# Kernel tuning notes

Hardware: AMD Instinct MI355X
Metric: run time of the kernel (lower is better)

The kernel has to match this reference:

```python
import jax, jax.numpy as jnp
import numpy as np

N_NODES = 100000
N_EDGES = 800000
# (in_dim, out_channels_per_head, heads) for the 5 stacked GATConv layers
DIMS = [(32, 24, 10), (240, 24, 5), (120, 24, 2), (48, 24, 1), (24, 12, 1)]
NEG_SLOPE = 0.2  # PyG GATConv default leaky_relu slope


def setup_inputs() -> dict:
    key = jax.random.key(0)
    ks = jax.random.split(key, 4 + 4 * len(DIMS))
    x = jax.random.normal(ks[0], (N_NODES, 32), jnp.float32)
    # edge_index with no self loops (dst = src + nonzero offset mod N),
    # since PyG GATConv removes then re-adds self loops.
    src = jax.random.randint(ks[1], (N_EDGES,), 0, N_NODES)
    off = jax.random.randint(ks[2], (N_EDGES,), 1, N_NODES)
    dst = (src + off) % N_NODES
    edge_index = jnp.stack([src, dst]).astype(jnp.int32)
    edge_attr = jax.random.normal(ks[3], (N_EDGES, 4), jnp.float32)
    inp = {"x": x, "edge_index": edge_index, "edge_attr": edge_attr}
    for i, (din, c, h) in enumerate(DIMS):
        kw, kb, ka, kd = ks[4 + 4 * i: 8 + 4 * i]
        s = 1.0 / np.sqrt(din)
        inp[f"W{i}"] = jax.random.normal(kw, (din, h * c), jnp.float32) * s
        inp[f"b{i}"] = jax.random.normal(kb, (h * c,), jnp.float32) * 0.01
        inp[f"as{i}"] = jax.random.normal(ka, (h, c), jnp.float32) * (1.0 / np.sqrt(c))
        inp[f"ad{i}"] = jax.random.normal(kd, (h, c), jnp.float32) * (1.0 / np.sqrt(c))
    return inp


def gat_layer(x, src, dst, W, b, a_src, a_dst):
    # Faithful PyG GATConv (concat=True, bias=True, edge_dim=None)
    n = x.shape[0]
    h_heads, c = a_src.shape
    h = (x @ W).reshape(n, h_heads, c)                      # [N,H,C]
    alpha_s = jnp.einsum('nhc,hc->nh', h, a_src)            # [N,H]
    alpha_d = jnp.einsum('nhc,hc->nh', h, a_dst)            # [N,H]
    e = jax.nn.leaky_relu(alpha_s[src] + alpha_d[dst], NEG_SLOPE)  # [E,H]
    # segment softmax over incoming edges of each destination node
    m = jax.ops.segment_max(e, dst, num_segments=n)         # [N,H]
    ex = jnp.exp(e - m[dst])
    z = jax.ops.segment_sum(ex, dst, num_segments=n)        # [N,H]
    attn = ex / z[dst]                                      # [E,H]
    out = jax.ops.segment_sum(h[src] * attn[:, :, None], dst, num_segments=n)
    return out.reshape(n, h_heads * c) + b


def reference(x, edge_index, edge_attr,
              W0, b0, as0, ad0, W1, b1, as1, ad1, W2, b2, as2, ad2,
              W3, b3, as3, ad3, W4, b4, as4, ad4):
    # edge_attr is ignored: GATConv(edge_dim=None) does not use it.
    n = x.shape[0]
    loop = jnp.arange(n, dtype=edge_index.dtype)
    src = jnp.concatenate([edge_index[0], loop])  # add self loops (PyG default)
    dst = jnp.concatenate([edge_index[1], loop])
    params = [(W0, b0, as0, ad0), (W1, b1, as1, ad1), (W2, b2, as2, ad2),
              (W3, b3, as3, ad3), (W4, b4, as4, ad4)]
    for W, b, a_s, a_d in params:
        x = jax.nn.relu(gat_layer(x, src, dst, W, b, a_s, a_d))
    return x
```

## Files before the change

kernel.cpp:

```cpp
#include <hip/hip_runtime.h>
#include <math.h>

#define NN 100000
#define EE 800000
#define ET (EE + NN)
#define BS 256
#define BKTS 391
#define FB_EPB 4096
#define LDSCAP 4096
#define DBINS 64

typedef _Float16 f16;
typedef __attribute__((ext_vector_type(2))) _Float16 h2v;
typedef __attribute__((ext_vector_type(4))) _Float16 half4;
typedef __attribute__((ext_vector_type(8))) _Float16 half8;
typedef __attribute__((ext_vector_type(4))) float f32x4;
template<int V> struct HV;
template<> struct HV<4>{ typedef half4 type; };
template<> struct HV<8>{ typedef half8 type; };

static inline int cdiv(long a, int b){ return (int)((a + b - 1) / b); }

__global__ __launch_bounds__(256) void k_bhist(const int* __restrict__ ei,
                                               int* __restrict__ bucketCount){
    __shared__ int hist[BKTS];
    for (int t = threadIdx.x; t < BKTS; t += 256) hist[t] = 0;
    __syncthreads();
    const int e0 = blockIdx.x * FB_EPB + threadIdx.x;
    #pragma unroll
    for (int i = 0; i < 16; i++){
        int e = e0 + i * 256;
        if (e < ET){
            int d = (e < EE) ? ei[EE + e] : (e - EE);
            atomicAdd(&hist[d >> 8], 1);
        }
    }
    __syncthreads();
    for (int t = threadIdx.x; t < BKTS; t += 256){
        int c = hist[t];
        if (c) atomicAdd(&bucketCount[t], c);
    }
}

__global__ void k_bscan(const int* __restrict__ bucketCount, int* __restrict__ bucketBase,
                        int* __restrict__ bucketCursor, int* __restrict__ rowptr){
    __shared__ int sh[512];
    int t = threadIdx.x;
    int c = (t < BKTS) ? bucketCount[t] : 0;
    sh[t] = c;
    __syncthreads();
    for (int o = 1; o < 512; o <<= 1){
        int v = (t >= o) ? sh[t - o] : 0;
        __syncthreads();
        sh[t] += v;
        __syncthreads();
    }
    if (t < BKTS){
        int excl = sh[t] - c;
        bucketBase[t] = excl;
        bucketCursor[t] = excl;
    }
    if (t == 0){
        bucketBase[BKTS] = ET;
        rowptr[NN] = ET;
    }
}

__global__ __launch_bounds__(256) void k_bfill(const int* __restrict__ ei,
        int* __restrict__ bucketCursor, unsigned* __restrict__ bpack){
    __shared__ int hist[BKTS];
    __shared__ int base[BKTS];
    for (int t = threadIdx.x; t < BKTS; t += 256) hist[t] = 0;
    __syncthreads();
    const int e0 = blockIdx.x * FB_EPB + threadIdx.x;
    unsigned pk[16], rb[16];
    #pragma unroll
    for (int i = 0; i < 16; i++){
        int e = e0 + i * 256;
        rb[i] = 0xFFFFFFFFu;
        if (e < ET){
            int s, d;
            if (e < EE){ s = ei[e]; d = ei[EE + e]; } else { s = e - EE; d = s; }
            int b = d >> 8;
            int r = atomicAdd(&hist[b], 1);
            pk[i] = ((unsigned)(d & 255) << 17) | (unsigned)s;
            rb[i] = ((unsigned)r << 9) | (unsigned)b;
        }
    }
    __syncthreads();
    for (int t = threadIdx.x; t < BKTS; t += 256){
        int c = hist[t];
        base[t] = c ? atomicAdd(&bucketCursor[t], c) : 0;
    }
    __syncthreads();
    #pragma unroll
    for (int i = 0; i < 16; i++){
        if (rb[i] != 0xFFFFFFFFu){
            int b = rb[i] & 511;
            int r = rb[i] >> 9;
            bpack[base[b] + r] = pk[i];
        }
    }
}

__global__ __launch_bounds__(256) void k_bsort(const unsigned* __restrict__ bpack,
        const int* __restrict__ bucketBase, int* __restrict__ rowptr,
        int* __restrict__ ssrc){
    __shared__ int cnt[256];
    __shared__ int off[256];
    __shared__ unsigned stage[LDSCAP];
    int b = blockIdx.x;
    int n0 = bucketBase[b], n1 = bucketBase[b + 1];
    int nE = n1 - n0;
    int t = threadIdx.x;
    cnt[t] = 0;
    __syncthreads();
    for (int i = t; i < nE; i += 256){
        unsigned v = bpack[n0 + i];
        atomicAdd(&cnt[v >> 17], 1);
    }
    __syncthreads();
    int cv = cnt[t];
    off[t] = cv;
    __syncthreads();
    for (int o = 1; o < 256; o <<= 1){
        int v = (t >= o) ? off[t - o] : 0;
        __syncthreads();
        off[t] += v;
        __syncthreads();
    }
    int excl = off[t] - cv;
    __syncthreads();
    off[t] = excl;
    cnt[t] = 0;
    __syncthreads();
    for (int i = t; i < nE; i += 256){
        unsigned v = bpack[n0 + i];
        int dl = v >> 17;
        int r = atomicAdd(&cnt[dl], 1);
        stage[off[dl] + r] = v;
    }
    int d = b * 256 + t;
    if (d < NN) rowptr[d] = n0 + excl;
    __syncthreads();
    for (int i = t; i < nE; i += 256){
        unsigned v = stage[i];
        ssrc[n0 + i] = (int)(v & 0x1FFFFu);
    }
}

__global__ __launch_bounds__(256) void k_dhist(const int* __restrict__ rowptr,
                                               int* __restrict__ dcnt){
    __shared__ int h[DBINS];
    int t = threadIdx.x;
    if (t < DBINS) h[t] = 0;
    __syncthreads();
    int n = blockIdx.x * 256 + t;
    if (n < NN){
        int d = rowptr[n + 1] - rowptr[n];
        if (d > DBINS - 1) d = DBINS - 1;
        atomicAdd(&h[d], 1);
    }
    __syncthreads();
    if (t < DBINS && h[t]) atomicAdd(&dcnt[t], h[t]);
}

__global__ void k_dscan(const int* __restrict__ dcnt, int* __restrict__ dcur){
    __shared__ int sh[DBINS];
    int t = threadIdx.x;
    sh[t] = dcnt[t];
    __syncthreads();
    int off = 0;
    for (int b = t + 1; b < DBINS; ++b) off += sh[b];
    dcur[t] = off;
}

__global__ __launch_bounds__(256) void k_dfill(const int* __restrict__ rowptr,
        int* __restrict__ dcur, int* __restrict__ perm){
    __shared__ int h[DBINS];
    __shared__ int base[DBINS];
    int t = threadIdx.x;
    if (t < DBINS) h[t] = 0;
    __syncthreads();
    int n = blockIdx.x * 256 + t;
    int d = 0, r = 0;
    if (n < NN){
        d = rowptr[n + 1] - rowptr[n];
        if (d > DBINS - 1) d = DBINS - 1;
        r = atomicAdd(&h[d], 1);
    }
    __syncthreads();
    if (t < DBINS){
        int c = h[t];
        base[t] = c ? atomicAdd(&dcur[t], c) : 0;
    }
    __syncthreads();
    if (n < NN) perm[base[d] + r] = n;
}

template<int K, int M, int KP, int MP, int HH, int CC>
__device__ __forceinline__ void prep_one(int idx, const float* __restrict__ W,
        const float* __restrict__ b, const float* __restrict__ as_,
        const float* __restrict__ ad_, f16* __restrict__ Wpk,
        float* __restrict__ bp, float* __restrict__ Was, float* __restrict__ Wad){
    constexpr int NT = MP / 16;
    if (idx < KP * MP){
        int j    = idx & 7;
        int lane = (idx >> 3) & 63;
        int rest = idx >> 9;
        int nt   = rest % NT;
        int ks   = rest / NT;
        int k = ks * 32 + ((lane >> 4) & 3) * 8 + j;
        int n = nt * 16 + (lane & 15);
        Wpk[idx] = (k < K && n < M) ? (f16)W[k * M + n] : (f16)0.f;
    }
    if (idx < MP) bp[idx] = (idx < M) ? b[idx] : 0.f;
    if (idx < K * HH){
        int k = idx / HH, hd = idx - k * HH;
        float s = 0.f, d = 0.f;
        #pragma unroll
        for (int c = 0; c < CC; c++){
            float w = W[k * M + hd * CC + c];
            s = fmaf(w, as_[hd * CC + c], s);
            d = fmaf(w, ad_[hd * CC + c], d);
        }
        Was[idx] = s;
        Wad[idx] = d;
    }
}

__device__ __forceinline__ void prep_w0(int idx, const float* __restrict__ W0,
                                        f16* __restrict__ Wpk0){
    int j    = idx & 7;
    int lane = (idx >> 3) & 63;
    int nt   = (idx >> 9) & 1;
    int hd   = idx >> 10;
    int k    = ((lane >> 4) & 3) * 8 + j;
    int cih  = nt * 16 + (lane & 15);
    Wpk0[idx] = (cih < 24) ? (f16)W0[k * 240 + hd * 24 + cih] : (f16)0.f;
}

struct PrepAll {
    const float *W[5], *b[5], *as[5], *ad[5];
    f16*   Wpk[5];
    f16*   Wpk0;
    float* bp[5];
    float* Was[5];
    float* Wad[5];
    int*   bucketCount;
    int*   dcnt;
};

__global__ void k_prep_all(PrepAll a){
    int idx = blockIdx.x * 256 + threadIdx.x;
    if (idx < 7680)
        prep_one< 32, 240,  32, 240, 10, 24>(idx,         a.W[0], a.b[0], a.as[0], a.ad[0], a.Wpk[0], a.bp[0], a.Was[0], a.Wad[0]);
    else if (idx < 40448)
        prep_one<240, 120, 256, 128,  5, 24>(idx - 7680,  a.W[1], a.b[1], a.as[1], a.ad[1], a.Wpk[1], a.bp[1], a.Was[1], a.Wad[1]);
    else if (idx < 48640)
        prep_one<120,  48, 128,  64,  2, 24>(idx - 40448, a.W[2], a.b[2], a.as[2], a.ad[2], a.Wpk[2], a.bp[2], a.Was[2], a.Wad[2]);
    else if (idx < 50688)
        prep_one< 48,  24,  64,  32,  1, 24>(idx - 48640, a.W[3], a.b[3], a.as[3], a.ad[3], a.Wpk[3], a.bp[3], a.Was[3], a.Wad[3]);
    else if (idx < 51200)
        prep_one< 24,  12,  32,  16,  1, 12>(idx - 50688, a.W[4], a.b[4], a.as[4], a.ad[4], a.Wpk[4], a.bp[4], a.Was[4], a.Wad[4]);
    else if (idx < 61440)
        prep_w0(idx - 51200, a.W[0], a.Wpk0);
    else if (idx < 61440 + BKTS)
        a.bucketCount[idx - 61440] = 0;
    else if (idx < 61440 + BKTS + DBINS)
        a.dcnt[idx - 61440 - BKTS] = 0;
}

__global__ void k_cvt_alpha0(const float* __restrict__ X, f16* __restrict__ Xh,
                             const float* __restrict__ Was, const float* __restrict__ Wad,
                             float* __restrict__ als, float* __restrict__ ald){
    int n = blockIdx.x * BS + threadIdx.x;
    if (n >= NN) return;
    float xr[32];
    #pragma unroll
    for (int i = 0; i < 8; i++){
        float4 v = *(const float4*)(X + (long)n * 32 + i * 4);
        xr[i * 4 + 0] = v.x; xr[i * 4 + 1] = v.y;
        xr[i * 4 + 2] = v.z; xr[i * 4 + 3] = v.w;
    }
    #pragma unroll
    for (int i = 0; i < 4; i++){
        half8 h;
        #pragma unroll
        for (int c = 0; c < 8; c++) h[c] = (f16)xr[i * 8 + c];
        *(half8*)(Xh + (long)n * 32 + i * 8) = h;
    }
    float s[10] = {}, d[10] = {};
    for (int k = 0; k < 32; k++){
        float x = xr[k];
        #pragma unroll
        for (int hd = 0; hd < 10; hd++){
            s[hd] = fmaf(x, Was[k * 10 + hd], s[hd]);
            d[hd] = fmaf(x, Wad[k * 10 + hd], d[hd]);
        }
    }
    #pragma unroll
    for (int hd = 0; hd < 10; hd++){
        als[(long)n * 12 + hd] = s[hd];
        ald[(long)n * 12 + hd] = d[hd];
    }
}

template<int MPH, int HH, int CC, int SL>
__global__ void k_alpha_h(const f16* __restrict__ H2, const float* __restrict__ as_,
                          const float* __restrict__ ad_, float* __restrict__ als,
                          float* __restrict__ ald){
    int n = blockIdx.x * BS + threadIdx.x;
    if (n >= NN) return;
    const f16* h = H2 + (long)n * MPH;
    #pragma unroll
    for (int hd = 0; hd < HH; hd++){
        float s = 0.f, d = 0.f;
        #pragma unroll
        for (int c0 = 0; c0 < CC; c0 += 4){
            half4 hv = *(const half4*)(h + hd * CC + c0);
            #pragma unroll
            for (int j = 0; j < 4; j++){
                float hvf = (float)hv[j];
                s = fmaf(hvf, as_[hd * CC + c0 + j], s);
                d = fmaf(hvf, ad_[hd * CC + c0 + j], d);
            }
        }
        als[(long)n * SL + hd] = s;
        ald[(long)n * SL + hd] = d;
    }
}

__device__ __forceinline__ void smx_upd(float& ma, float& L, float& z, float e, float adv){
    float mn = fmaxf(ma, e);
    float Ln = mn + adv; Ln = (Ln >= 0.f) ? Ln : 0.2f * Ln;
    float ev = e + adv;  ev = (ev >= 0.f) ? ev : 0.2f * ev;
    z = z * __expf(L - Ln) + __expf(ev - Ln);
    ma = mn; L = Ln;
}

template<int HH, int SL, int ATTS, int TPN>
__global__ __launch_bounds__(256) void k_mzatt_split(const float* __restrict__ als,
        const float* __restrict__ ald, const int* __restrict__ rowptr,
        const int* __restrict__ ssrc, f16* __restrict__ att){
    constexpr int HPT = HH / TPN;
    long idx = (long)blockIdx.x * 256 + threadIdx.x;
    if (idx >= (long)NN * TPN) return;
    int n = (int)(idx / TPN);
    int g = (int)(idx - (long)n * TPN);
    const int c0 = g * HPT;
    float adv[HPT], ma[HPT], L[HPT], z[HPT];
    #pragma unroll
    for (int h = 0; h < HPT; h++){
        adv[h] = ald[(long)n * SL + c0 + h];
        ma[h] = -1e30f; L[h] = -1e30f; z[h] = 0.f;
    }
    const int beg = rowptr[n], end = rowptr[n + 1];
    int p = beg;
    for (; p + 4 <= end; p += 4){
        int s0 = ssrc[p], s1 = ssrc[p+1], s2 = ssrc[p+2], s3 = ssrc[p+3];
        float e0[HPT], e1[HPT], e2[HPT], e3[HPT];
        if constexpr (HPT == 2){
            float2 v0 = *(const float2*)(als + (long)s0 * SL + c0);
            float2 v1 = *(const float2*)(als + (long)s1 * SL + c0);
            float2 v2 = *(const float2*)(als + (long)s2 * SL + c0);
            float2 v3 = *(const float2*)(als + (long)s3 * SL + c0);
            e0[0]=v0.x; e0[1]=v0.y; e1[0]=v1.x; e1[1]=v1.y;
            e2[0]=v2.x; e2[1]=v2.y; e3[0]=v3.x; e3[1]=v3.y;
        } else {
            e0[0] = als[(long)s0 * SL + c0];
            e1[0] = als[(long)s1 * SL + c0];
            e2[0] = als[(long)s2 * SL + c0];
            e3[0] = als[(long)s3 * SL + c0];
        }
        #pragma unroll
        for (int h = 0; h < HPT; h++){
            smx_upd(ma[h], L[h], z[h], e0[h], adv[h]);
            smx_upd(ma[h], L[h], z[h], e1[h], adv[h]);
            smx_upd(ma[h], L[h], z[h], e2[h], adv[h]);
            smx_upd(ma[h], L[h], z[h], e3[h], adv[h]);
        }
    }
    for (; p < end; ++p){
        int s = ssrc[p];
        float e[HPT];
        if constexpr (HPT == 2){
            float2 v = *(const float2*)(als + (long)s * SL + c0);
            e[0] = v.x; e[1] = v.y;
        } else {
            e[0] = als[(long)s * SL + c0];
        }
        #pragma unroll
        for (int h = 0; h < HPT; h++) smx_upd(ma[h], L[h], z[h], e[h], adv[h]);
    }
    float zi[HPT];
    int pos[HPT];
    #pragma unroll
    for (int h = 0; h < HPT; h++){
        zi[h] = 1.f / z[h];
        int hh = c0 + h;
        pos[h] = (ATTS == 16) ? (hh + ((hh >= 5) ? 3 : 0)) : hh;
    }
    auto emit = [&](int pp, const float* e){
        #pragma unroll
        for (int h = 0; h < HPT; h++){
            float ev = e[h] + adv[h]; ev = (ev >= 0.f) ? ev : 0.2f * ev;
            att[(long)pp * ATTS + pos[h]] = (f16)(__expf(ev - L[h]) * zi[h]);
        }
    };
    p = beg;
    for (; p + 4 <= end; p += 4){
        int s0 = ssrc[p], s1 = ssrc[p+1], s2 = ssrc[p+2], s3 = ssrc[p+3];
        float e0[HPT], e1[HPT], e2[HPT], e3[HPT];
        if constexpr (HPT == 2){
            float2 v0 = *(const float2*)(als + (long)s0 * SL + c0);
            float2 v1 = *(const float2*)(als + (long)s1 * SL + c0);
            float2 v2 = *(const float2*)(als + (long)s2 * SL + c0);
            float2 v3 = *(const float2*)(als + (long)s3 * SL + c0);
            e0[0]=v0.x; e0[1]=v0.y; e1[0]=v1.x; e1[1]=v1.y;
            e2[0]=v2.x; e2[1]=v2.y; e3[0]=v3.x; e3[1]=v3.y;
        } else {
            e0[0] = als[(long)s0 * SL + c0];
            e1[0] = als[(long)s1 * SL + c0];
            e2[0] = als[(long)s2 * SL + c0];
            e3[0] = als[(long)s3 * SL + c0];
        }
        emit(p, e0); emit(p+1, e1); emit(p+2, e2); emit(p+3, e3);
    }
    for (; p < end; ++p){
        int s = ssrc[p];
        float e[HPT];
        if constexpr (HPT == 2){
            float2 v = *(const float2*)(als + (long)s * SL + c0);
            e[0] = v.x; e[1] = v.y;
        } else {
            e[0] = als[(long)s * SL + c0];
        }
        emit(p, e);
    }
}

__global__ __launch_bounds__(256) void k_aggX0_gemm(const f16* __restrict__ Xh,
        const f16* __restrict__ att, const int* __restrict__ rowptr,
        const int* __restrict__ ssrc, const int* __restrict__ perm,
        const f16* __restrict__ Wpk0, const float* __restrict__ bp0,
        f16* __restrict__ X1){
    constexpr int SA = 328;
    constexpr int SO = 264;
    __shared__ f16 smem[32 * SA];
    const int t = threadIdx.x;
    const int n0 = blockIdx.x * 32;

    {
        const int nloc = t >> 3;
        const int hg   = (t >> 2) & 1;
        const int ch   = t & 3;
        const int n    = perm[n0 + nloc];
        float acc[5][8] = {};
        int beg = rowptr[n], end = rowptr[n + 1];
        int p = beg;
        for (; p + 4 <= end; p += 4){
            int s0 = ssrc[p], s1 = ssrc[p+1], s2 = ssrc[p+2], s3 = ssrc[p+3];
            half8 x0 = *(const half8*)(Xh + (long)s0 * 32 + ch * 8);
            half8 x1 = *(const half8*)(Xh + (long)s1 * 32 + ch * 8);
            half8 x2 = *(const half8*)(Xh + (long)s2 * 32 + ch * 8);
            half8 x3 = *(const half8*)(Xh + (long)s3 * 32 + ch * 8);
            half8 a0 = *(const half8*)(att + (long)p * 16 + hg * 8);
            half8 a1 = *(const half8*)(att + (long)(p+1) * 16 + hg * 8);
            half8 a2 = *(const half8*)(att + (long)(p+2) * 16 + hg * 8);
            half8 a3 = *(const half8*)(att + (long)(p+3) * 16 + hg * 8);
            #pragma unroll
            for (int h = 0; h < 5; h++){
                float w0 = (float)a0[h], w1 = (float)a1[h];
                float w2 = (float)a2[h], w3 = (float)a3[h];
                #pragma unroll
                for (int c = 0; c < 8; c++){
                    acc[h][c] = fmaf(w0, (float)x0[c], acc[h][c]);
                    acc[h][c] = fmaf(w1, (float)x1[c], acc[h][c]);
                    acc[h][c] = fmaf(w2, (float)x2[c], acc[h][c]);
                    acc[h][c] = fmaf(w3, (float)x3[c], acc[h][c]);
                }
            }
        }
        for (; p < end; ++p){
            int s = ssrc[p];
            half8 xv = *(const half8*)(Xh + (long)s * 32 + ch * 8);
            half8 av = *(const half8*)(att + (long)p * 16 + hg * 8);
            #pragma unroll
            for (int h = 0; h < 5; h++){
                float w = (float)av[h];
                #pragma unroll
                for (int c = 0; c < 8; c++)
                    acc[h][c] = fmaf(w, (float)xv[c], acc[h][c]);
            }
        }
        #pragma unroll
        for (int h = 0; h < 5; h++){
            half8 o;
            #pragma unroll
            for (int c = 0; c < 8; c++) o[c] = (f16)acc[h][c];
            *(half8*)(smem + nloc * SA + (hg * 5 + h) * 32 + ch * 8) = o;
        }
    }
    __syncthreads();

    const int wave = t >> 6;
    const int lane = t & 63;
    const int quad = lane >> 4;
    const int l16  = lane & 15;
    const int mt   = wave & 1;
    half8 afr[5];
    #pragma unroll
    for (int i = 0; i < 5; i++){
        const int hd = (wave + 4 * i) >> 1;
        afr[i] = *(const half8*)(smem + (mt * 16 + l16) * SA + hd * 32 + quad * 8);
    }
    __syncthreads();
    #pragma unroll
    for (int i = 0; i < 5; i++){
        const int hd = (wave + 4 * i) >> 1;
        #pragma unroll
        for (int nt = 0; nt < 2; nt++){
            half8 bfr = *(const half8*)(Wpk0 + ((hd * 2 + nt) * 64 + lane) * 8);
            f32x4 acc2 = (f32x4){0.f, 0.f, 0.f, 0.f};
            acc2 = __builtin_amdgcn_mfma_f32_16x16x32_f16(afr[i], bfr, acc2, 0, 0, 0);
            int cih = nt * 16 + l16;
            if (cih < 24){
                float bv = bp0[hd * 24 + cih];
                #pragma unroll
                for (int reg = 0; reg < 4; reg++){
                    int rl = mt * 16 + quad * 4 + reg;
                    float v = acc2[reg] + bv;
                    smem[rl * SO + hd * 24 + cih] = (f16)((v > 0.f) ? v : 0.f);
                }
            }
        }
    }
    __syncthreads();

    const half8 hz = {};
    #pragma unroll
    for (int c = t; c < 1024; c += 256){
        int row = c >> 5, c8 = c & 31;
        long rn = perm[n0 + row];
        half8 v = (c8 >= 30) ? hz : *(const half8*)(smem + row * SO + c8 * 8);
        *(half8*)(X1 + rn * 256 + c8 * 8) = v;
    }
}

template<int KP, int MPH>
__global__ __launch_bounds__(256) void k_gemm_mfma(const f16* __restrict__ Xh,
        const f16* __restrict__ Wpk, f16* __restrict__ H2){
    constexpr int NT = MPH / 16;
    constexpr int KS = KP / 32;
    const int wave = threadIdx.x >> 6;
    const int lane = threadIdx.x & 63;
    const int quad = lane >> 4;
    const int l16  = lane & 15;
    const long row0 = (long)blockIdx.x * 128 + wave * 32;

    f32x4 acc[2][NT];
    #pragma unroll
    for (int mt = 0; mt < 2; mt++)
        #pragma unroll
        for (int nt = 0; nt < NT; nt++)
            acc[mt][nt] = (f32x4){0.f, 0.f, 0.f, 0.f};

    const long r0 = row0 + l16;
    const long r1 = row0 + 16 + l16;
    const half8 hz = {};
    half8 a0 = (r0 < NN) ? *(const half8*)(Xh + r0 * KP + quad * 8) : hz;
    half8 a1 = (r1 < NN) ? *(const half8*)(Xh + r1 * KP + quad * 8) : hz;
    half8 bc[NT];
    #pragma unroll
    for (int nt = 0; nt < NT; nt++)
        bc[nt] = *(const half8*)(Wpk + ((long)nt * 64 + lane) * 8);

    for (int ks = 0; ks < KS; ks++){
        half8 n0 = hz, n1 = hz, bn[NT];
        if (ks + 1 < KS){
            const int kk = (ks + 1) * 32 + quad * 8;
            n0 = (r0 < NN) ? *(const half8*)(Xh + r0 * KP + kk) : hz;
            n1 = (r1 < NN) ? *(const half8*)(Xh + r1 * KP + kk) : hz;
            const f16* bp_ = Wpk + ((long)(ks + 1) * NT * 64 + lane) * 8;
            #pragma unroll
            for (int nt = 0; nt < NT; nt++)
                bn[nt] = *(const half8*)(bp_ + (long)nt * 512);
        } else {
            #pragma unroll
            for (int nt = 0; nt < NT; nt++) bn[nt] = hz;
        }
        #pragma unroll
        for (int nt = 0; nt < NT; nt++){
            acc[0][nt] = __builtin_amdgcn_mfma_f32_16x16x32_f16(a0, bc[nt], acc[0][nt], 0, 0, 0);
            acc[1][nt] = __builtin_amdgcn_mfma_f32_16x16x32_f16(a1, bc[nt], acc[1][nt], 0, 0, 0);
        }
        a0 = n0; a1 = n1;
        #pragma unroll
        for (int nt = 0; nt < NT; nt++) bc[nt] = bn[nt];
    }
    #pragma unroll
    for (int mt = 0; mt < 2; mt++){
        #pragma unroll
        for (int reg = 0; reg < 4; reg++){
            long r = row0 + mt * 16 + quad * 4 + reg;
            if (r < NN){
                #pragma unroll
                for (int nt = 0; nt < NT; nt++)
                    H2[r * MPH + nt * 16 + l16] = (f16)acc[mt][nt][reg];
            }
        }
    }
}

template<int HH, int CC, int ATTS, int MPH, int MPO, int VEC, bool O16>
__global__ __launch_bounds__(256) void k_agg_h(const f16* __restrict__ H2,
        const f16* __restrict__ att,
        const int* __restrict__ rowptr, const int* __restrict__ ssrc,
        const float* __restrict__ bp, f16* __restrict__ out16,
        float* __restrict__ out32, int MREAL){
    constexpr int TPN = MPO / VEC;
    typedef typename HV<VEC>::type hvec;
    int idx = blockIdx.x * 256 + threadIdx.x;
    if (idx >= NN * TPN) return;
    int n = idx / TPN;
    int q = idx - n * TPN;
    int j0 = q * VEC;
    if constexpr (O16 && (MPO > MPH)){
        if (j0 >= MPH){
            hvec zv = {};
            *(hvec*)(out16 + (long)n * MPO + j0) = zv;
            return;
        }
    }
    int hd = j0 / CC; if (hd > HH - 1) hd = HH - 1;

    int beg = rowptr[n], end = rowptr[n + 1];
    float acc[VEC] = {};
    int p = beg;
    for (; p + 4 <= end; p += 4){
        int s0 = ssrc[p], s1 = ssrc[p+1], s2 = ssrc[p+2], s3 = ssrc[p+3];
        float w0 = (float)att[(long)p * ATTS + hd];
        float w1 = (float)att[(long)(p+1) * ATTS + hd];
        float w2 = (float)att[(long)(p+2) * ATTS + hd];
        float w3 = (float)att[(long)(p+3) * ATTS + hd];
        hvec h0 = *(const hvec*)(H2 + (long)s0 * MPH + j0);
        hvec h1 = *(const hvec*)(H2 + (long)s1 * MPH + j0);
        hvec h2 = *(const hvec*)(H2 + (long)s2 * MPH + j0);
        hvec h3 = *(const hvec*)(H2 + (long)s3 * MPH + j0);
        #pragma unroll
        for (int c = 0; c < VEC; c++){
            acc[c] = fmaf(w0, (float)h0[c], acc[c]);
            acc[c] = fmaf(w1, (float)h1[c], acc[c]);
            acc[c] = fmaf(w2, (float)h2[c], acc[c]);
            acc[c] = fmaf(w3, (float)h3[c], acc[c]);
        }
    }
    for (; p < end; ++p){
        int s = ssrc[p];
        float w = (float)att[(long)p * ATTS + hd];
        hvec hv = *(const hvec*)(H2 + (long)s * MPH + j0);
        #pragma unroll
        for (int c = 0; c < VEC; c++)
            acc[c] = fmaf(w, (float)hv[c], acc[c]);
    }
    if constexpr (O16){
        hvec o;
        #pragma unroll
        for (int c = 0; c < VEC; c++){
            float v = acc[c] + bp[j0 + c];
            o[c] = (f16)((v > 0.f) ? v : 0.f);
        }
        *(hvec*)(out16 + (long)n * MPO + j0) = o;
    } else {
        if (j0 < MREAL){
            #pragma unroll
            for (int c = 0; c < VEC; c++){
                float v = acc[c] + bp[j0 + c];
                out32[(long)n * MREAL + j0 + c] = (v > 0.f) ? v : 0.f;
            }
        }
    }
}

template<int K, int M, int KP, int MPH, int MPO, int HH, int CC, int ATTS, int VEC,
         bool O16, int SL, int TPN>
static void run_layer(const f16* Xin, f16* H2, f16* att,
                      const f16* Wpk, const float* bp,
                      const float* asv, const float* adv,
                      float* als, float* ald,
                      const int* rowptr, const int* ssrc,
                      f16* Xnext, float* out32, hipStream_t stream){
    constexpr int OTPN = MPO / VEC;
    k_gemm_mfma<KP, MPH><<<cdiv(NN, 128), 256, 0, stream>>>(Xin, Wpk, H2);
    k_alpha_h<MPH, HH, CC, SL><<<cdiv(NN, BS), BS, 0, stream>>>(H2, asv, adv, als, ald);
    k_mzatt_split<HH, SL, ATTS, TPN><<<cdiv((long)NN * TPN, 256), 256, 0, stream>>>(
        als, ald, rowptr, ssrc, att);
    k_agg_h<HH, CC, ATTS, MPH, MPO, VEC, O16><<<cdiv((long)NN * OTPN, 256), 256, 0, stream>>>(
        H2, att, rowptr, ssrc, bp, Xnext, out32, M);
}

extern "C" void kernel_launch(void* const* d_in, const int* in_sizes, int n_in,
                              void* d_out, int out_size, void* d_ws, size_t ws_size,
                              hipStream_t stream){
    const float* x0 = (const float*)d_in[0];
    const int*   ei = (const int*)d_in[1];
    PrepAll pa;
    for (int i = 0; i < 5; i++){
        pa.W[i]  = (const float*)d_in[3 + 4 * i];
        pa.b[i]  = (const float*)d_in[4 + 4 * i];
        pa.as[i] = (const float*)d_in[5 + 4 * i];
        pa.ad[i] = (const float*)d_in[6 + 4 * i];
    }

    char* p = (char*)d_ws;
    auto alloc = [&](size_t bytes) -> char* {
        char* r = p;
        p += (bytes + 255) & ~(size_t)255;
        return r;
    };
    f16*   Xh     = (f16*)alloc((size_t)NN * 256 * 2);
    f16*   H2     = (f16*)alloc((size_t)NN * 320 * 2);
    f16*   att    = (f16*)alloc((size_t)ET * 16 * 2);
    float* als    = (float*)alloc((size_t)NN * 12 * 4);
    float* ald    = (float*)alloc((size_t)NN * 12 * 4);
    const int wpkSz[5] = {7680, 32768, 8192, 2048, 512};
    const int mpSz[5]  = {240, 128, 64, 32, 16};
    const int khSz[5]  = {320, 1200, 240, 48, 24};
    for (int i = 0; i < 5; i++){
        pa.Wpk[i] = (f16*)alloc((size_t)wpkSz[i] * 2);
        pa.bp[i]  = (float*)alloc((size_t)mpSz[i] * 4);
        pa.Was[i] = (float*)alloc((size_t)khSz[i] * 4);
        pa.Wad[i] = (float*)alloc((size_t)khSz[i] * 4);
    }
    pa.Wpk0 = (f16*)alloc((size_t)10240 * 2);
    int*      bucketCount  = (int*)alloc((size_t)BKTS * 4);
    int*      bucketBase   = (int*)alloc((size_t)(BKTS + 1) * 4);
    int*      bucketCursor = (int*)alloc((size_t)BKTS * 4);
    unsigned* bpack        = (unsigned*)alloc((size_t)ET * 4);
    int*      rowptr       = (int*)alloc((size_t)(NN + 1) * 4);
    int*      ssrc         = (int*)alloc((size_t)ET * 4);
    int*      dcnt         = (int*)alloc((size_t)DBINS * 4);
    int*      dcur         = (int*)alloc((size_t)DBINS * 4);
    int*      perm         = (int*)alloc((size_t)NN * 4);
    pa.bucketCount = bucketCount;
    pa.dcnt = dcnt;

    k_prep_all<<<242, 256, 0, stream>>>(pa);
    k_bhist<<<cdiv(ET, FB_EPB), 256, 0, stream>>>(ei, bucketCount);
    k_bscan<<<1, 512, 0, stream>>>(bucketCount, bucketBase, bucketCursor, rowptr);
    k_bfill<<<cdiv(ET, FB_EPB), 256, 0, stream>>>(ei, bucketCursor, bpack);
    k_bsort<<<BKTS, 256, 0, stream>>>(bpack, bucketBase, rowptr, ssrc);
    k_dhist<<<cdiv(NN, 256), 256, 0, stream>>>(rowptr, dcnt);
    k_dscan<<<1, DBINS, 0, stream>>>(dcnt, dcur);
    k_dfill<<<cdiv(NN, 256), 256, 0, stream>>>(rowptr, dcur, perm);

    k_cvt_alpha0<<<cdiv(NN, BS), BS, 0, stream>>>(x0, Xh, pa.Was[0], pa.Wad[0], als, ald);
    k_mzatt_split<10, 12, 16, 5><<<cdiv((long)NN * 5, 256), 256, 0, stream>>>(
        als, ald, rowptr, ssrc, att);
    k_aggX0_gemm<<<NN / 32, 256, 0, stream>>>(Xh, att, rowptr, ssrc, perm,
        pa.Wpk0, pa.bp[0], H2 );

    run_layer<240, 120, 256, 128, 128,  5, 24, 8, 8, true,  8, 5>(H2, Xh, att, pa.Wpk[1],
        pa.bp[1], pa.as[1], pa.ad[1], als, ald, rowptr, ssrc, H2, nullptr, stream);
    run_layer<120,  48, 128,  64,  64,  2, 24, 2, 8, true,  2, 2>(H2, Xh, att, pa.Wpk[2],
        pa.bp[2], pa.as[2], pa.ad[2], als, ald, rowptr, ssrc, H2, nullptr, stream);
    run_layer< 48,  24,  64,  32,  32,  1, 24, 1, 8, true,  1, 1>(H2, Xh, att, pa.Wpk[3],
        pa.bp[3], pa.as[3], pa.ad[3], als, ald, rowptr, ssrc, H2, nullptr, stream);
    run_layer< 24,  12,  32,  16,  16,  1, 12, 1, 4, false, 1, 1>(H2, Xh, att, pa.Wpk[4],
        pa.bp[4], pa.as[4], pa.ad[4], als, ald, rowptr, ssrc, nullptr, (float*)d_out, stream);
}
```

Baseline: 465.0 us.

## Fuse segment softmax into aggregation and parallelize alpha projection for later layers

For layers 1-4, the separate softmax kernel that wrote per-edge attention weights is removed. The aggregation kernel now recomputes the online max and normalizer per node and head from the alpha values, then recomputes the weights while gathering features. This drops the attention write and re-read and one launch per layer, at the cost of every channel-group thread redoing the softmax gathers. The alpha projection now splits each node across threads and reduces in shared memory, and the degree histogram is folded into the bucket sort kernel so the k_dhist launch goes away.

```diff
diff --git a/kernel.cpp b/kernel.cpp
--- a/kernel.cpp
+++ b/kernel.cpp
@@ -11,7 +11,6 @@
 #define DBINS 64
 
 typedef _Float16 f16;
-typedef __attribute__((ext_vector_type(2))) _Float16 h2v;
 typedef __attribute__((ext_vector_type(4))) _Float16 half4;
 typedef __attribute__((ext_vector_type(8))) _Float16 half8;
 typedef __attribute__((ext_vector_type(4))) float f32x4;
@@ -105,7 +104,7 @@
 
 __global__ __launch_bounds__(256) void k_bsort(const unsigned* __restrict__ bpack,
         const int* __restrict__ bucketBase, int* __restrict__ rowptr,
-        int* __restrict__ ssrc){
+        int* __restrict__ ssrc, int* __restrict__ dcnt){
     __shared__ int cnt[256];
     __shared__ int off[256];
     __shared__ unsigned stage[LDSCAP];
@@ -141,28 +140,16 @@
         stage[off[dl] + r] = v;
     }
     int d = b * 256 + t;
-    if (d < NN) rowptr[d] = n0 + excl;
+    if (d < NN){
+        rowptr[d] = n0 + excl;
+        int dg = (cv > DBINS - 1) ? (DBINS - 1) : cv;
+        atomicAdd(&dcnt[dg], 1);
+    }
     __syncthreads();
     for (int i = t; i < nE; i += 256){
         unsigned v = stage[i];
         ssrc[n0 + i] = (int)(v & 0x1FFFFu);
     }
-}
-
-__global__ __launch_bounds__(256) void k_dhist(const int* __restrict__ rowptr,
-                                               int* __restrict__ dcnt){
-    __shared__ int h[DBINS];
-    int t = threadIdx.x;
-    if (t < DBINS) h[t] = 0;
-    __syncthreads();
-    int n = blockIdx.x * 256 + t;
-    if (n < NN){
-        int d = rowptr[n + 1] - rowptr[n];
-        if (d > DBINS - 1) d = DBINS - 1;
-        atomicAdd(&h[d], 1);
-    }
-    __syncthreads();
-    if (t < DBINS && h[t]) atomicAdd(&dcnt[t], h[t]);
 }
 
 __global__ void k_dscan(const int* __restrict__ dcnt, int* __restrict__ dcur){
@@ -306,28 +293,50 @@
     }
 }
 
-template<int MPH, int HH, int CC, int SL>
-__global__ void k_alpha_h(const f16* __restrict__ H2, const float* __restrict__ as_,
-                          const float* __restrict__ ad_, float* __restrict__ als,
-                          float* __restrict__ ald){
-    int n = blockIdx.x * BS + threadIdx.x;
-    if (n >= NN) return;
-    const f16* h = H2 + (long)n * MPH;
-    #pragma unroll
-    for (int hd = 0; hd < HH; hd++){
-        float s = 0.f, d = 0.f;
-        #pragma unroll
-        for (int c0 = 0; c0 < CC; c0 += 4){
-            half4 hv = *(const half4*)(h + hd * CC + c0);
+template<int MPH, int M, int HH, int CC, int SL>
+__global__ __launch_bounds__(256) void k_alpha_v2(const f16* __restrict__ H2,
+        const float* __restrict__ as_, const float* __restrict__ ad_,
+        float* __restrict__ als, float* __restrict__ ald){
+    constexpr int TA  = MPH / 8;
+    constexpr int NPB = 256 / TA;
+    __shared__ float sAs[256], sAd[256], sBs[256], sBd[256];
+    const int t  = threadIdx.x;
+    const int nl = t / TA;
+    const int c  = t - nl * TA;
+    const long n = (long)blockIdx.x * NPB + nl;
+    float pAs = 0.f, pAd = 0.f, pBs = 0.f, pBd = 0.f;
+    if (n < NN){
+        half8 hv = *(const half8*)(H2 + n * MPH + c * 8);
+        const int j0 = c * 8;
+        const int hA = j0 / CC;
+        const int sp = (hA + 1) * CC - j0;
+        #pragma unroll
+        for (int i = 0; i < 8; i++){
+            int j = j0 + i;
+            float w  = (float)hv[i];
+            float ws = (j < M) ? as_[j] : 0.f;
+            float wd = (j < M) ? ad_[j] : 0.f;
+            if (i < sp){ pAs = fmaf(w, ws, pAs); pAd = fmaf(w, wd, pAd); }
+            else       { pBs = fmaf(w, ws, pBs); pBd = fmaf(w, wd, pBd); }
+        }
+    }
+    sAs[t] = pAs; sAd[t] = pAd; sBs[t] = pBs; sBd[t] = pBd;
+    __syncthreads();
+    if (t < NPB * HH){
+        int nl2 = t / HH, hd = t - nl2 * HH;
+        long n2 = (long)blockIdx.x * NPB + nl2;
+        if (n2 < NN){
+            float s = 0.f, d = 0.f;
             #pragma unroll
-            for (int j = 0; j < 4; j++){
-                float hvf = (float)hv[j];
-                s = fmaf(hvf, as_[hd * CC + c0 + j], s);
-                d = fmaf(hvf, ad_[hd * CC + c0 + j], d);
+            for (int c2 = 0; c2 < TA; c2++){
+                int j0 = c2 * 8, hA = j0 / CC, sp = (hA + 1) * CC - j0;
+                int base = nl2 * TA + c2;
+                if (hA == hd){ s += sAs[base]; d += sAd[base]; }
+                if (sp < 8 && hA + 1 == hd){ s += sBs[base]; d += sBd[base]; }
             }
-        }
-        als[(long)n * SL + hd] = s;
-        ald[(long)n * SL + hd] = d;
+            als[n2 * SL + hd] = s;
+            ald[n2 * SL + hd] = d;
+        }
     }
 }
 
@@ -401,33 +410,7 @@
         int hh = c0 + h;
         pos[h] = (ATTS == 16) ? (hh + ((hh >= 5) ? 3 : 0)) : hh;
     }
-    auto emit = [&](int pp, const float* e){
-        #pragma unroll
-        for (int h = 0; h < HPT; h++){
-            float ev = e[h] + adv[h]; ev = (ev >= 0.f) ? ev : 0.2f * ev;
-            att[(long)pp * ATTS + pos[h]] = (f16)(__expf(ev - L[h]) * zi[h]);
-        }
-    };
-    p = beg;
-    for (; p + 4 <= end; p += 4){
-        int s0 = ssrc[p], s1 = ssrc[p+1], s2 = ssrc[p+2], s3 = ssrc[p+3];
-        float e0[HPT], e1[HPT], e2[HPT], e3[HPT];
-        if constexpr (HPT == 2){
-            float2 v0 = *(const float2*)(als + (long)s0 * SL + c0);
-            float2 v1 = *(const float2*)(als + (long)s1 * SL + c0);
-            float2 v2 = *(const float2*)(als + (long)s2 * SL + c0);
-            float2 v3 = *(const float2*)(als + (long)s3 * SL + c0);
-            e0[0]=v0.x; e0[1]=v0.y; e1[0]=v1.x; e1[1]=v1.y;
-            e2[0]=v2.x; e2[1]=v2.y; e3[0]=v3.x; e3[1]=v3.y;
-        } else {
-            e0[0] = als[(long)s0 * SL + c0];
-            e1[0] = als[(long)s1 * SL + c0];
-            e2[0] = als[(long)s2 * SL + c0];
-            e3[0] = als[(long)s3 * SL + c0];
-        }
-        emit(p, e0); emit(p+1, e1); emit(p+2, e2); emit(p+3, e3);
-    }
-    for (; p < end; ++p){
+    for (p = beg; p < end; ++p){
         int s = ssrc[p];
         float e[HPT];
         if constexpr (HPT == 2){
@@ -436,7 +419,11 @@
         } else {
             e[0] = als[(long)s * SL + c0];
         }
-        emit(p, e);
+        #pragma unroll
+        for (int h = 0; h < HPT; h++){
+            float ev = e[h] + adv[h]; ev = (ev >= 0.f) ? ev : 0.2f * ev;
+            att[(long)p * ATTS + pos[h]] = (f16)(__expf(ev - L[h]) * zi[h]);
+        }
     }
 }
 
@@ -613,37 +600,57 @@
     }
 }
 
-template<int HH, int CC, int ATTS, int MPH, int MPO, int VEC, bool O16>
-__global__ __launch_bounds__(256) void k_agg_h(const f16* __restrict__ H2,
-        const f16* __restrict__ att,
+template<int HH, int CC, int MPH, int MPO, int VEC, bool O16, int SL>
+__global__ __launch_bounds__(256) void k_aggsm_h(const f16* __restrict__ H2,
+        const float* __restrict__ als, const float* __restrict__ ald,
         const int* __restrict__ rowptr, const int* __restrict__ ssrc,
         const float* __restrict__ bp, f16* __restrict__ out16,
         float* __restrict__ out32, int MREAL){
     constexpr int TPN = MPO / VEC;
     typedef typename HV<VEC>::type hvec;
-    int idx = blockIdx.x * 256 + threadIdx.x;
-    if (idx >= NN * TPN) return;
-    int n = idx / TPN;
-    int q = idx - n * TPN;
+    long idx = (long)blockIdx.x * 256 + threadIdx.x;
+    if (idx >= (long)NN * TPN) return;
+    int n = (int)(idx / TPN);
+    int q = (int)(idx - (long)n * TPN);
     int j0 = q * VEC;
-    if constexpr (O16 && (MPO > MPH)){
-        if (j0 >= MPH){
-            hvec zv = {};
-            *(hvec*)(out16 + (long)n * MPO + j0) = zv;
-            return;
-        }
-    }
+    if constexpr (!O16){ if (j0 >= MREAL) return; }
     int hd = j0 / CC; if (hd > HH - 1) hd = HH - 1;
-
-    int beg = rowptr[n], end = rowptr[n + 1];
-    float acc[VEC] = {};
+    const float adv = ald[(long)n * SL + hd];
+    const int beg = rowptr[n], end = rowptr[n + 1];
+
+    float ma = -1e30f, L = -1e30f, z = 0.f;
     int p = beg;
     for (; p + 4 <= end; p += 4){
         int s0 = ssrc[p], s1 = ssrc[p+1], s2 = ssrc[p+2], s3 = ssrc[p+3];
-        float w0 = (float)att[(long)p * ATTS + hd];
-        float w1 = (float)att[(long)(p+1) * ATTS + hd];
-        float w2 = (float)att[(long)(p+2) * ATTS + hd];
-        float w3 = (float)att[(long)(p+3) * ATTS + hd];
+        float e0 = als[(long)s0 * SL + hd];
+        float e1 = als[(long)s1 * SL + hd];
+        float e2 = als[(long)s2 * SL + hd];
+        float e3 = als[(long)s3 * SL + hd];
+        smx_upd(ma, L, z, e0, adv);
+        smx_upd(ma, L, z, e1, adv);
+        smx_upd(ma, L, z, e2, adv);
+        smx_upd(ma, L, z, e3, adv);
+    }
+    for (; p < end; ++p)
+        smx_upd(ma, L, z, als[(long)ssrc[p] * SL + hd], adv);
+    const float zi = 1.f / z;
+
+    float acc[VEC] = {};
+    p = beg;
+    for (; p + 4 <= end; p += 4){
+        int s0 = ssrc[p], s1 = ssrc[p+1], s2 = ssrc[p+2], s3 = ssrc[p+3];
+        float e0 = als[(long)s0 * SL + hd];
+        float e1 = als[(long)s1 * SL + hd];
+        float e2 = als[(long)s2 * SL + hd];
+        float e3 = als[(long)s3 * SL + hd];
+        e0 += adv; e0 = (e0 >= 0.f) ? e0 : 0.2f * e0;
+        e1 += adv; e1 = (e1 >= 0.f) ? e1 : 0.2f * e1;
+        e2 += adv; e2 = (e2 >= 0.f) ? e2 : 0.2f * e2;
+        e3 += adv; e3 = (e3 >= 0.f) ? e3 : 0.2f * e3;
+        float w0 = __expf(e0 - L) * zi;
+        float w1 = __expf(e1 - L) * zi;
+        float w2 = __expf(e2 - L) * zi;
+        float w3 = __expf(e3 - L) * zi;
         hvec h0 = *(const hvec*)(H2 + (long)s0 * MPH + j0);
         hvec h1 = *(const hvec*)(H2 + (long)s1 * MPH + j0);
         hvec h2 = *(const hvec*)(H2 + (long)s2 * MPH + j0);
@@ -658,7 +665,9 @@
     }
     for (; p < end; ++p){
         int s = ssrc[p];
-        float w = (float)att[(long)p * ATTS + hd];
+        float e = als[(long)s * SL + hd] + adv;
+        e = (e >= 0.f) ? e : 0.2f * e;
+        float w = __expf(e - L) * zi;
         hvec hv = *(const hvec*)(H2 + (long)s * MPH + j0);
         #pragma unroll
         for (int c = 0; c < VEC; c++)
@@ -673,31 +682,28 @@
         }
         *(hvec*)(out16 + (long)n * MPO + j0) = o;
     } else {
-        if (j0 < MREAL){
-            #pragma unroll
-            for (int c = 0; c < VEC; c++){
-                float v = acc[c] + bp[j0 + c];
-                out32[(long)n * MREAL + j0 + c] = (v > 0.f) ? v : 0.f;
-            }
-        }
-    }
-}
-
-template<int K, int M, int KP, int MPH, int MPO, int HH, int CC, int ATTS, int VEC,
-         bool O16, int SL, int TPN>
-static void run_layer(const f16* Xin, f16* H2, f16* att,
+        #pragma unroll
+        for (int c = 0; c < VEC; c++){
+            float v = acc[c] + bp[j0 + c];
+            out32[(long)n * MREAL + j0 + c] = (v > 0.f) ? v : 0.f;
+        }
+    }
+}
+
+template<int K, int M, int KP, int MPH, int MPO, int HH, int CC, int VEC, bool O16, int SL>
+static void run_layer(const f16* Xin, f16* H2,
                       const f16* Wpk, const float* bp,
                       const float* asv, const float* adv,
                       float* als, float* ald,
                       const int* rowptr, const int* ssrc,
                       f16* Xnext, float* out32, hipStream_t stream){
     constexpr int OTPN = MPO / VEC;
+    constexpr int TA = MPH / 8;
     k_gemm_mfma<KP, MPH><<<cdiv(NN, 128), 256, 0, stream>>>(Xin, Wpk, H2);
-    k_alpha_h<MPH, HH, CC, SL><<<cdiv(NN, BS), BS, 0, stream>>>(H2, asv, adv, als, ald);
-    k_mzatt_split<HH, SL, ATTS, TPN><<<cdiv((long)NN * TPN, 256), 256, 0, stream>>>(
-        als, ald, rowptr, ssrc, att);
-    k_agg_h<HH, CC, ATTS, MPH, MPO, VEC, O16><<<cdiv((long)NN * OTPN, 256), 256, 0, stream>>>(
-        H2, att, rowptr, ssrc, bp, Xnext, out32, M);
+    k_alpha_v2<MPH, M, HH, CC, SL><<<cdiv((long)NN * TA, 256), 256, 0, stream>>>(
+        H2, asv, adv, als, ald);
+    k_aggsm_h<HH, CC, MPH, MPO, VEC, O16, SL><<<cdiv((long)NN * OTPN, 256), 256, 0, stream>>>(
+        H2, als, ald, rowptr, ssrc, bp, Xnext, out32, M);
 }
 
 extern "C" void kernel_launch(void* const* d_in, const int* in_sizes, int n_in,
@@ -750,8 +756,7 @@
     k_bhist<<<cdiv(ET, FB_EPB), 256, 0, stream>>>(ei, bucketCount);
     k_bscan<<<1, 512, 0, stream>>>(bucketCount, bucketBase, bucketCursor, rowptr);
     k_bfill<<<cdiv(ET, FB_EPB), 256, 0, stream>>>(ei, bucketCursor, bpack);
-    k_bsort<<<BKTS, 256, 0, stream>>>(bpack, bucketBase, rowptr, ssrc);
-    k_dhist<<<cdiv(NN, 256), 256, 0, stream>>>(rowptr, dcnt);
+    k_bsort<<<BKTS, 256, 0, stream>>>(bpack, bucketBase, rowptr, ssrc, dcnt);
     k_dscan<<<1, DBINS, 0, stream>>>(dcnt, dcur);
     k_dfill<<<cdiv(NN, 256), 256, 0, stream>>>(rowptr, dcur, perm);
 
@@ -761,12 +766,12 @@
     k_aggX0_gemm<<<NN / 32, 256, 0, stream>>>(Xh, att, rowptr, ssrc, perm,
         pa.Wpk0, pa.bp[0], H2 );
 
-    run_layer<240, 120, 256, 128, 128,  5, 24, 8, 8, true,  8, 5>(H2, Xh, att, pa.Wpk[1],
+    run_layer<240, 120, 256, 128, 128,  5, 24, 8, true,  8>(H2, Xh, pa.Wpk[1],
         pa.bp[1], pa.as[1], pa.ad[1], als, ald, rowptr, ssrc, H2, nullptr, stream);
-    run_layer<120,  48, 128,  64,  64,  2, 24, 2, 8, true,  2, 2>(H2, Xh, att, pa.Wpk[2],
+    run_layer<120,  48, 128,  64,  64,  2, 24, 8, true,  2>(H2, Xh, pa.Wpk[2],
         pa.bp[2], pa.as[2], pa.ad[2], als, ald, rowptr, ssrc, H2, nullptr, stream);
-    run_layer< 48,  24,  64,  32,  32,  1, 24, 1, 8, true,  1, 1>(H2, Xh, att, pa.Wpk[3],
+    run_layer< 48,  24,  64,  32,  32,  1, 24, 8, true,  1>(H2, Xh, pa.Wpk[3],
         pa.bp[3], pa.as[3], pa.ad[3], als, ald, rowptr, ssrc, H2, nullptr, stream);
-    run_layer< 24,  12,  32,  16,  16,  1, 12, 1, 4, false, 1, 1>(H2, Xh, att, pa.Wpk[4],
+    run_layer< 24,  12,  32,  16,  16,  1, 12, 4, false, 1>(H2, Xh, pa.Wpk[4],
         pa.bp[4], pa.as[4], pa.ad[4], als, ald, rowptr, ssrc, nullptr, (float*)d_out, stream);
 }
```

New measurement: 824.9 us. 77.4% more time.
